# Kernel tuning notes

Measured on AMD Instinct MI355X. Metric: run time of the kernel, lower is better.

## Reference

```python
import math
import jax, jax.numpy as jnp
import numpy as np

B, S, D, H = 2, 2048, 2048, 16
HD = D // H  # 128
EPS = 1e-5


def setup_inputs() -> dict:
    key = jax.random.key(0)
    ks = jax.random.split(key, 7)
    x = jax.random.normal(ks[0], (B, S, D), jnp.float32)
    # RoPE tables: (seqlen, head_dim//2)
    theta = 10000.0
    inv_freq = 1.0 / (theta ** (np.arange(0, HD, 2, dtype=np.float32) / HD))
    t = np.arange(S, dtype=np.float32)
    freqs = np.outer(t, inv_freq)  # (S, HD//2)
    freqs_cos = jnp.asarray(np.cos(freqs), jnp.float32)
    freqs_sin = jnp.asarray(np.sin(freqs), jnp.float32)
    sc = 0.02
    wq = jax.random.normal(ks[1], (D, D), jnp.float32) * sc  # stored (in, out)
    wk = jax.random.normal(ks[2], (D, D), jnp.float32) * sc
    wv = jax.random.normal(ks[3], (D, D), jnp.float32) * sc
    wu = jax.random.normal(ks[4], (D, D), jnp.float32) * sc
    wo = jax.random.normal(ks[5], (D, D), jnp.float32) * sc
    norm_w = jnp.ones((D,), jnp.float32)
    return {"x": x, "freqs_cos": freqs_cos, "freqs_sin": freqs_sin,
            "wq": wq, "wk": wk, "wv": wv, "wu": wu, "wo": wo, "norm_w": norm_w}


def _rope(t, cos, sin):
    # t: (B, S, H, HD); cos/sin: (S, HD//2)
    tr = t.reshape(t.shape[:-1] + (-1, 2))
    r, i = tr[..., 0], tr[..., 1]
    c = cos[None, :, None, :]
    s = sin[None, :, None, :]
    out_r = r * c - i * s
    out_i = r * s + i * c
    return jnp.stack([out_r, out_i], axis=-1).reshape(t.shape)


def reference(x, freqs_cos, freqs_sin, wq, wk, wv, wu, wo, norm_w):
    b, s, d = x.shape
    h = jax.nn.silu(x)  # pre-projection SiLU on the input
    q = (h @ wq).reshape(b, s, H, HD)
    k = (h @ wk).reshape(b, s, H, HD)
    v = (h @ wv).reshape(b, s, H, HD)
    u = h @ wu  # reshape->transpose->flatten in original is identity on (b,s,d)
    q = _rope(q, freqs_cos, freqs_sin)
    k = _rope(k, freqs_cos, freqs_sin)
    # scores: (b, H, s, s)
    scores = jnp.einsum('bqhd,bkhd->bhqk', q, k) / math.sqrt(HD)
    causal = jnp.tril(jnp.ones((s, s), bool))  # mask!=0 positions zeroed; silu(0)=0
    scores = jnp.where(causal[None, None], jax.nn.silu(scores), 0.0)
    out = jnp.einsum('bhqk,bkhd->bqhd', scores, v).reshape(b, s, d)
    # RMSNorm
    out = out * jax.lax.rsqrt(jnp.mean(out * out, axis=-1, keepdims=True) + EPS)
    out = out * norm_w
    out = out * u
    return out @ wo
```

## Files before the change

### kernel.cpp

```cpp
#include <hip/hip_runtime.h>
#include <hip/hip_bf16.h>
#include <cstdint>

typedef __attribute__((ext_vector_type(8))) short bf16x8;
typedef __attribute__((ext_vector_type(4))) float f32x4;
typedef unsigned short u16;

constexpr int B = 2, S = 2048, D = 2048, H = 16, HD = 128;
constexpr int M = B * S;
constexpr int NQKU = 6144;
constexpr int ATT_LD = 3072;
constexpr float SCALE = 0.08838834764831845f;

static __device__ __forceinline__ float b2f(u16 u) {
    union { float f; uint32_t i; } v; v.i = ((uint32_t)u) << 16; return v.f;
}
static __device__ __forceinline__ u16 f2b(float f) {
    union { float f; uint32_t i; } v; v.f = f;
    uint32_t x = v.i;
    return (u16)((x + 0x7FFFu + ((x >> 16) & 1u)) >> 16);
}

__device__ __forceinline__ void gll16(const void* g, void* l) {
    __builtin_amdgcn_global_load_lds(
        (const __attribute__((address_space(1))) uint32_t*)g,
        (__attribute__((address_space(3))) uint32_t*)l, 16, 0, 0);
}

#define BAR() do { asm volatile("" ::: "memory"); __builtin_amdgcn_s_barrier(); \
                   asm volatile("" ::: "memory"); } while (0)

__global__ __launch_bounds__(256) void silu_cast(const float* __restrict__ x,
                                                 u16* __restrict__ h, int n) {
    int i = (blockIdx.x * 256 + threadIdx.x) * 4;
    if (i >= n) return;
    float4 v = *(const float4*)(x + i);
    ushort4 o;
    o.x = f2b(v.x / (1.f + __expf(-v.x)));
    o.y = f2b(v.y / (1.f + __expf(-v.y)));
    o.z = f2b(v.z / (1.f + __expf(-v.z)));
    o.w = f2b(v.w / (1.f + __expf(-v.w)));
    *(ushort4*)(h + i) = o;
}

__global__ __launch_bounds__(256) void wcast(const float* __restrict__ w,
                                             u16* __restrict__ wT) {
    __shared__ float t[64][65];
    int tx = threadIdx.x & 63, ty = threadIdx.x >> 6;
    int kb = blockIdx.y * 64, nb = blockIdx.x * 64;
    for (int r = ty; r < 64; r += 4)
        t[r][tx] = w[(size_t)(kb + r) * D + nb + tx];
    __syncthreads();
    for (int r = ty; r < 64; r += 4)
        wT[(size_t)(nb + r) * D + kb + tx] = f2b(t[tx][r]);
}

__global__ __launch_bounds__(512, 2)
void gemm_qkuv(const u16* __restrict__ A, const u16* __restrict__ BT,
               u16* __restrict__ qku, u16* __restrict__ vt) {
    __shared__ u16 lds[65536];
    const int tid = threadIdx.x;
    const int lane = tid & 63, wid = tid >> 6;
    const int wm = wid >> 2, wn = wid & 3;
    const int l16 = lane & 15, lq = lane >> 4;

    const int orig = blockIdx.x;
    const int swz = (orig & 7) * 64 + (orig >> 3);
    const int mt = swz & 15, nt = swz >> 4;
    const int m0 = mt * 256, n0 = nt * 256;

    const int srow = tid >> 2;
    const int ce = ((tid & 3) * 8) ^ (((tid >> 5) & 1) << 4);
    const int rdx = (lq * 16) ^ (((l16 >> 3) & 1) << 5);

    const u16* As0 = A + (size_t)(m0 + srow) * D + ce;
    const u16* Bs0 = BT + (size_t)(n0 + srow) * D + ce;

    {
        u16* dA = lds + wid * 512;
        u16* dB = lds + 16384 + wid * 512;
        gll16(As0,                    dA);
        gll16(As0 + (size_t)128 * D,  dA + 8192);
        gll16(Bs0,                    dB);
        gll16(Bs0 + (size_t)128 * D,  dB + 8192);
        gll16(As0 + 32,                    dA + 4096);
        gll16(As0 + 32 + (size_t)128 * D,  dA + 8192 + 4096);
        gll16(Bs0 + 32,                    dB + 4096);
        gll16(Bs0 + 32 + (size_t)128 * D,  dB + 8192 + 4096);
    }
    asm volatile("s_waitcnt vmcnt(4)" ::: "memory");
    BAR();

    f32x4 acc[8][4] = {};
    bf16x8 a[8];
    const int rbB = (wn & 1) * 4096;

#define LOAD_A(kk)                                                            \
    _Pragma("unroll") for (int mi = 0; mi < 8; ++mi)                          \
        a[mi] = *(const bf16x8*)(Abase + (kk) * 8192 +                        \
                                 (mi * 16 + l16) * 64 + rdx);
#define LOAD_B(dst, nia, kk)                                                  \
    dst = *(const bf16x8*)(Bbase + (kk) * 8192 + rbB +                        \
                           ((nia) * 16 + l16) * 64 + rdx);
#define MFMA2(n0i, n1i)                                                       \
    __builtin_amdgcn_s_setprio(1);                                            \
    _Pragma("unroll") for (int mi = 0; mi < 8; ++mi) {                        \
        acc[mi][n0i] = __builtin_amdgcn_mfma_f32_16x16x32_bf16(a[mi], b0,     \
                            acc[mi][n0i], 0, 0, 0);                           \
        acc[mi][n1i] = __builtin_amdgcn_mfma_f32_16x16x32_bf16(a[mi], b1,     \
                            acc[mi][n1i], 0, 0, 0);                           \
    }                                                                          \
    __builtin_amdgcn_s_setprio(0);

    for (int kt = 0; kt < 32; ++kt) {
        const int buf = kt & 1;
        const char* Abase = (const char*)lds + buf * 65536 + wm * 16384;
        const char* Bbase = (const char*)lds + 32768 + buf * 65536 + (wn >> 1) * 16384;
        const bool st = (kt + 1) < 32;
        const u16* Asrc = As0 + (kt + 1) * 64;
        const u16* Bsrc = Bs0 + (kt + 1) * 64;
        u16* dA = lds + (buf ^ 1) * 32768 + wid * 512;
        u16* dB = dA + 16384;
        bf16x8 b0, b1;

        LOAD_A(0);
        LOAD_B(b0, 0, 0);
        LOAD_B(b1, 1, 0);
        if (st) { gll16(Asrc, dA); gll16(Asrc + (size_t)128 * D, dA + 8192); }
        BAR();
        MFMA2(0, 1);
        BAR();
        LOAD_B(b0, 2, 0);
        LOAD_B(b1, 3, 0);
        if (st) { gll16(Bsrc, dB); gll16(Bsrc + (size_t)128 * D, dB + 8192); }
        BAR();
        MFMA2(2, 3);
        if (kt == 31) asm volatile("s_waitcnt vmcnt(0)" ::: "memory");
        else         asm volatile("s_waitcnt vmcnt(4)" ::: "memory");
        BAR();
        LOAD_A(1);
        LOAD_B(b0, 0, 1);
        LOAD_B(b1, 1, 1);
        if (st) { gll16(Asrc + 32, dA + 4096); gll16(Asrc + 32 + (size_t)128 * D, dA + 8192 + 4096); }
        BAR();
        MFMA2(0, 1);
        BAR();
        LOAD_B(b0, 2, 1);
        LOAD_B(b1, 3, 1);
        if (st) { gll16(Bsrc + 32, dB + 4096); gll16(Bsrc + 32 + (size_t)128 * D, dB + 8192 + 4096); }
        BAR();
        MFMA2(2, 3);
        if (kt < 31) asm volatile("s_waitcnt vmcnt(4)" ::: "memory");
        BAR();
    }
#undef LOAD_A
#undef LOAD_B
#undef MFMA2

    if (n0 >= NQKU) {
#pragma unroll
        for (int mi = 0; mi < 8; ++mi)
#pragma unroll
            for (int ni = 0; ni < 4; ++ni) {
                int c = n0 - NQKU + wn * 64 + ni * 16 + l16;
                int hh = c >> 7, d = c & 127;
                int row0 = m0 + wm * 128 + mi * 16 + lq * 4;
                int bb = row0 >> 11, s0 = row0 & 2047;
                ushort4 pk = make_ushort4(f2b(acc[mi][ni][0]), f2b(acc[mi][ni][1]),
                                          f2b(acc[mi][ni][2]), f2b(acc[mi][ni][3]));
                *(ushort4*)(vt + (((size_t)(bb * H + hh) * HD + d) * S + s0)) = pk;
            }
    } else {
#pragma unroll
        for (int mi = 0; mi < 8; ++mi)
#pragma unroll
            for (int ni = 0; ni < 4; ++ni)
#pragma unroll
                for (int r = 0; r < 4; ++r) {
                    int row = m0 + wm * 128 + mi * 16 + lq * 4 + r;
                    int col = n0 + wn * 64 + ni * 16 + l16;
                    qku[(size_t)row * NQKU + col] = f2b(acc[mi][ni][r]);
                }
    }
}

__global__ __launch_bounds__(256)
void gemm_bt_f32(const u16* __restrict__ A, const u16* __restrict__ BT,
                 float* __restrict__ out, int lda, int ldc, int Kk) {
    __shared__ u16 As[128 * 32];
    __shared__ u16 Bs[128 * 32];
    const int tid = threadIdx.x;
    const int lane = tid & 63, w = tid >> 6;
    const int wm = w >> 1, wn = w & 1;
    const int l16 = lane & 15, lq = lane >> 4;
    const int m0 = blockIdx.y * 128, n0 = blockIdx.x * 128;
    const int rs = lane >> 2;
    const int cs = (lane & 3) * 8;
    f32x4 acc[4][4] = {};

    const u16* Ab = A + (size_t)(m0 + w * 32 + rs) * lda + cs;
    const u16* Bb = BT + (size_t)(n0 + w * 32 + rs) * Kk + cs;
    u16* Al = As + w * 32 * 32;
    u16* Bl = Bs + w * 32 * 32;

    for (int k0 = 0; k0 < Kk; k0 += 32) {
        gll16(Ab + k0, Al);
        gll16(Ab + k0 + (size_t)16 * lda, Al + 16 * 32);
        gll16(Bb + k0, Bl);
        gll16(Bb + k0 + (size_t)16 * Kk, Bl + 16 * 32);
        __syncthreads();
        bf16x8 af[4], bfr[4];
#pragma unroll
        for (int mi = 0; mi < 4; mi++)
            af[mi] = *(const bf16x8*)(As + (wm * 64 + mi * 16 + l16) * 32 + lq * 8);
#pragma unroll
        for (int ni = 0; ni < 4; ni++)
            bfr[ni] = *(const bf16x8*)(Bs + (wn * 64 + ni * 16 + l16) * 32 + lq * 8);
#pragma unroll
        for (int mi = 0; mi < 4; mi++)
#pragma unroll
            for (int ni = 0; ni < 4; ni++)
                acc[mi][ni] = __builtin_amdgcn_mfma_f32_16x16x32_bf16(
                    af[mi], bfr[ni], acc[mi][ni], 0, 0, 0);
        __syncthreads();
    }
#pragma unroll
    for (int mi = 0; mi < 4; mi++)
#pragma unroll
        for (int ni = 0; ni < 4; ni++)
#pragma unroll
            for (int r = 0; r < 4; r++) {
                int row = m0 + wm * 64 + mi * 16 + lq * 4 + r;
                int col = n0 + wn * 64 + ni * 16 + l16;
                out[(size_t)row * ldc + col] = acc[mi][ni][r];
            }
}

__global__ __launch_bounds__(256)
void reformat(const u16* __restrict__ qku, const float* __restrict__ fc,
              const float* __restrict__ fs, u16* __restrict__ qr,
              u16* __restrict__ kr) {
    int bh = blockIdx.x;
    int s0 = blockIdx.y * 64;
    int b = bh >> 4, h = bh & 15;
    int tid = threadIdx.x;
#pragma unroll
    for (int i = 0; i < 16; ++i) {
        int p = tid + i * 256;
        int row = p >> 6, pp = p & 63;
        int sgl = s0 + row;
        float c = fc[sgl * 64 + pp], sn = fs[sgl * 64 + pp];
        size_t src = (size_t)(b * S + sgl) * NQKU + h * HD + 2 * pp;
        size_t dst = ((size_t)bh * S + sgl) * HD + 2 * pp;
        {
            uint32_t qv = *(const uint32_t*)(qku + src);
            float r = b2f((u16)(qv & 0xffff)), im = b2f((u16)(qv >> 16));
            uint32_t o = (uint32_t)f2b(r * c - im * sn) |
                         ((uint32_t)f2b(r * sn + im * c) << 16);
            *(uint32_t*)(qr + dst) = o;
        }
        {
            uint32_t kv = *(const uint32_t*)(qku + src + 2048);
            float r = b2f((u16)(kv & 0xffff)), im = b2f((u16)(kv >> 16));
            uint32_t o = (uint32_t)f2b(r * c - im * sn) |
                         ((uint32_t)f2b(r * sn + im * c) << 16);
            *(uint32_t*)(kr + dst) = o;
        }
    }
}

__global__ __launch_bounds__(512, 2)
void hstu_attn(const u16* __restrict__ qr, const u16* __restrict__ kr,
               const u16* __restrict__ vt, float* __restrict__ att) {
    __shared__ u16 k_l[16384];
    __shared__ u16 v_l[16384];
    __shared__ u16 s_l[8 * 16 * 136];
    const int bh = blockIdx.x & 31, slot = blockIdx.x >> 5;
    const int b = bh >> 4, h = bh & 15;
    const int tid = threadIdx.x, lane = tid & 63, w = tid >> 6;
    const int l16 = lane & 15, lq = lane >> 4;
    u16* s_w = s_l + w * 16 * 136;

    const u16* kb = kr + (size_t)bh * S * HD;
    const u16* vb = vt + (size_t)bh * HD * S;

    const int irow0 = tid >> 4, iu0 = tid & 15;

#define STAGE_K(k0_)                                                          \
    _Pragma("unroll") for (int r_ = 0; r_ < 4; ++r_) {                        \
        int row_ = irow0 + r_ * 32;                                           \
        int uc_ = iu0 ^ (row_ & 7);                                           \
        gll16(kb + (size_t)(k0_ + row_) * HD + uc_ * 8,                       \
              k_l + ((w * 64 + r_ * 512) << 3));                              \
    }
#define STAGE_V(k0_)                                                          \
    _Pragma("unroll") for (int r_ = 0; r_ < 4; ++r_) {                        \
        int row_ = irow0 + r_ * 32;                                           \
        int uc_ = iu0 ^ (row_ & 7);                                           \
        gll16(vb + (size_t)row_ * S + (k0_) + uc_ * 8,                        \
              v_l + ((w * 64 + r_ * 512) << 3));                              \
    }

    for (int pass = 0; pass < 2; ++pass) {
        const int t = pass ? (15 - slot) : slot;
        const int q0 = t * 128;
        const int qg0 = q0 + w * 16;

        bf16x8 qf[4];
#pragma unroll
        for (int kk = 0; kk < 4; ++kk)
            qf[kk] = *(const bf16x8*)(qr + ((size_t)bh * S + qg0 + l16) * HD +
                                      kk * 32 + lq * 8);
        f32x4 acco[8] = {};

        STAGE_K(0);
        STAGE_V(0);
        asm volatile("s_waitcnt vmcnt(0)" ::: "memory");
        BAR();

        for (int kt = 0; kt <= t; ++kt) {
            const int k0 = kt * 128;
            const bool st = kt < t;
            f32x4 accs[8] = {};
            __builtin_amdgcn_s_setprio(1);
#pragma unroll
            for (int kk = 0; kk < 4; ++kk)
#pragma unroll
                for (int ni = 0; ni < 8; ++ni) {
                    int row = ni * 16 + l16;
                    bf16x8 kf = *(const bf16x8*)(k_l + row * 128 +
                                ((kk * 32 + lq * 8) ^ ((row & 7) << 3)));
                    accs[ni] = __builtin_amdgcn_mfma_f32_16x16x32_bf16(
                        qf[kk], kf, accs[ni], 0, 0, 0);
                }
            __builtin_amdgcn_s_setprio(0);
            const bool dg = (kt == t);
#pragma unroll
            for (int ni = 0; ni < 8; ++ni)
#pragma unroll
                for (int r = 0; r < 4; ++r) {
                    int qrow = lq * 4 + r;
                    int krow = ni * 16 + l16;
                    float vv = accs[ni][r] * SCALE;
                    vv = (!dg || (k0 + krow <= qg0 + qrow))
                             ? vv / (1.f + __expf(-vv)) : 0.f;
                    s_w[qrow * 136 + krow] = f2b(vv);
                }
            BAR();
            if (st) STAGE_K(k0 + 128);
            if (st) asm volatile("s_waitcnt vmcnt(4)" ::: "memory");
            else    asm volatile("s_waitcnt vmcnt(0)" ::: "memory");
            BAR();
            __builtin_amdgcn_s_setprio(1);
#pragma unroll
            for (int kk = 0; kk < 4; ++kk) {
                bf16x8 sf = *(const bf16x8*)(s_w + l16 * 136 + kk * 32 + lq * 8);
#pragma unroll
                for (int ni = 0; ni < 8; ++ni) {
                    int row = ni * 16 + l16;
                    bf16x8 vf = *(const bf16x8*)(v_l + row * 128 +
                                ((kk * 32 + lq * 8) ^ ((row & 7) << 3)));
                    acco[ni] = __builtin_amdgcn_mfma_f32_16x16x32_bf16(
                        sf, vf, acco[ni], 0, 0, 0);
                }
            }
            __builtin_amdgcn_s_setprio(0);
            BAR();
            if (st) {
                STAGE_V(k0 + 128);
                asm volatile("s_waitcnt vmcnt(4)" ::: "memory");
            }
            BAR();
        }
#pragma unroll
        for (int ni = 0; ni < 8; ++ni)
#pragma unroll
            for (int r = 0; r < 4; ++r)
                att[(size_t)(b * S + qg0 + lq * 4 + r) * ATT_LD +
                    h * HD + ni * 16 + l16] = acco[ni][r];
    }
#undef STAGE_K
#undef STAGE_V
}

__global__ __launch_bounds__(256)
void rms_mul(const float* __restrict__ att, u16* __restrict__ qku,
             const float* __restrict__ nw) {
    int row = blockIdx.x;
    int tid = threadIdx.x;
    const float* a = att + (size_t)row * ATT_LD + tid * 8;
    float4 v0 = *(const float4*)(a);
    float4 v1 = *(const float4*)(a + 4);
    float ss = v0.x * v0.x + v0.y * v0.y + v0.z * v0.z + v0.w * v0.w +
               v1.x * v1.x + v1.y * v1.y + v1.z * v1.z + v1.w * v1.w;
#pragma unroll
    for (int off = 32; off > 0; off >>= 1) ss += __shfl_down(ss, off, 64);
    __shared__ float red[4];
    int lane = tid & 63, w = tid >> 6;
    if (lane == 0) red[w] = ss;
    __syncthreads();
    float rs = rsqrtf((red[0] + red[1] + red[2] + red[3]) * (1.f / D) + 1e-5f);
    int col = tid * 8;
    u16* up = qku + (size_t)row * NQKU + 4096 + col;
    u16 ut[8];
    *(int4*)ut = *(const int4*)up;
    float f[8] = {v0.x, v0.y, v0.z, v0.w, v1.x, v1.y, v1.z, v1.w};
    u16 o[8];
#pragma unroll
    for (int j = 0; j < 8; j++)
        o[j] = f2b(f[j] * rs * nw[col + j] * b2f(ut[j]));
    *(int4*)up = *(int4*)o;
}

extern "C" void kernel_launch(void* const* d_in, const int* in_sizes, int n_in,
                              void* d_out, int out_size, void* d_ws, size_t ws_size,
                              hipStream_t stream) {
    const float* x  = (const float*)d_in[0];
    const float* fc = (const float*)d_in[1];
    const float* fs = (const float*)d_in[2];
    const float* wq = (const float*)d_in[3];
    const float* wk = (const float*)d_in[4];
    const float* wv = (const float*)d_in[5];
    const float* wu = (const float*)d_in[6];
    const float* wo = (const float*)d_in[7];
    const float* nw = (const float*)d_in[8];
    float* out = (float*)d_out;

    char* ws = (char*)d_ws;
    const size_t WSZ = (size_t)D * D * sizeof(u16);
    u16* h_b  = (u16*)(ws);
    u16* wT   = (u16*)(ws + 2 * WSZ);
    u16* qku  = (u16*)(ws + 7 * WSZ);
    u16* vt   = (u16*)(ws + 13 * WSZ);
    u16* k_r  = (u16*)(ws + 15 * WSZ);
    u16* q_r  = h_b;
    float* att = (float*)qku;

    silu_cast<<<M * D / 1024, 256, 0, stream>>>(x, h_b, M * D);
    dim3 wg(32, 32);
    wcast<<<wg, 256, 0, stream>>>(wq, wT + 0 * (size_t)D * D);
    wcast<<<wg, 256, 0, stream>>>(wk, wT + 1 * (size_t)D * D);
    wcast<<<wg, 256, 0, stream>>>(wu, wT + 2 * (size_t)D * D);
    wcast<<<wg, 256, 0, stream>>>(wv, wT + 3 * (size_t)D * D);
    wcast<<<wg, 256, 0, stream>>>(wo, wT + 4 * (size_t)D * D);

    gemm_qkuv<<<512, 512, 0, stream>>>(h_b, wT, qku, vt);

    reformat<<<dim3(32, 32), 256, 0, stream>>>(qku, fc, fs, q_r, k_r);
    hstu_attn<<<256, 512, 0, stream>>>(q_r, k_r, vt, att);
    rms_mul<<<M, 256, 0, stream>>>(att, qku, nw);
    gemm_bt_f32<<<dim3(D / 128, M / 128), 256, 0, stream>>>(
        qku + 4096, wT + 4 * (size_t)D * D, out, NQKU, D, D);
}
```

Before: 361.7 us.

## Retile attention waves into a 2x4 grid to reuse K/V fragments

The attention kernel's per-wave work changes from 16 query rows by 128 key columns to a 2x4 wave grid. Each wave now owns 64 query rows by 32 key columns, so each K/V fragment read from LDS feeds four MFMAs instead of one, cutting LDS read traffic per tile. The score tile becomes a single block-wide shared buffer instead of per-wave slices, and SiLU uses a hardware reciprocal instead of a division. In exchange, each wave holds four times as many Q fragments in registers, which raises register pressure under the 2-blocks-per-CU launch bound and risks lower occupancy or spills.

```diff
diff --git a/kernel.cpp b/kernel.cpp
--- a/kernel.cpp
+++ b/kernel.cpp
@@ -274,16 +274,15 @@
                const u16* __restrict__ vt, float* __restrict__ att) {
     __shared__ u16 k_l[16384];
     __shared__ u16 v_l[16384];
-    __shared__ u16 s_l[8 * 16 * 136];
+    __shared__ u16 s_l[128 * 136];
     const int bh = blockIdx.x & 31, slot = blockIdx.x >> 5;
     const int b = bh >> 4, h = bh & 15;
     const int tid = threadIdx.x, lane = tid & 63, w = tid >> 6;
     const int l16 = lane & 15, lq = lane >> 4;
-    u16* s_w = s_l + w * 16 * 136;
+    const int wq = w >> 2, wk4 = w & 3;
 
     const u16* kb = kr + (size_t)bh * S * HD;
     const u16* vb = vt + (size_t)bh * HD * S;
-
     const int irow0 = tid >> 4, iu0 = tid & 15;
 
 #define STAGE_K(k0_)                                                          \
@@ -304,14 +303,16 @@
     for (int pass = 0; pass < 2; ++pass) {
         const int t = pass ? (15 - slot) : slot;
         const int q0 = t * 128;
-        const int qg0 = q0 + w * 16;
-
-        bf16x8 qf[4];
-#pragma unroll
-        for (int kk = 0; kk < 4; ++kk)
-            qf[kk] = *(const bf16x8*)(qr + ((size_t)bh * S + qg0 + l16) * HD +
-                                      kk * 32 + lq * 8);
-        f32x4 acco[8] = {};
+
+        bf16x8 qf[4][4];
+#pragma unroll
+        for (int mi = 0; mi < 4; ++mi)
+#pragma unroll
+            for (int kk = 0; kk < 4; ++kk)
+                qf[mi][kk] = *(const bf16x8*)(qr +
+                    ((size_t)bh * S + q0 + wq * 64 + mi * 16 + l16) * HD +
+                    kk * 32 + lq * 8);
+        f32x4 acco[4][2] = {};
 
         STAGE_K(0);
         STAGE_V(0);
@@ -321,31 +322,36 @@
         for (int kt = 0; kt <= t; ++kt) {
             const int k0 = kt * 128;
             const bool st = kt < t;
-            f32x4 accs[8] = {};
+            f32x4 accs[4][2] = {};
             __builtin_amdgcn_s_setprio(1);
 #pragma unroll
             for (int kk = 0; kk < 4; ++kk)
 #pragma unroll
-                for (int ni = 0; ni < 8; ++ni) {
-                    int row = ni * 16 + l16;
+                for (int ni = 0; ni < 2; ++ni) {
+                    int row = wk4 * 32 + ni * 16 + l16;
                     bf16x8 kf = *(const bf16x8*)(k_l + row * 128 +
                                 ((kk * 32 + lq * 8) ^ ((row & 7) << 3)));
-                    accs[ni] = __builtin_amdgcn_mfma_f32_16x16x32_bf16(
-                        qf[kk], kf, accs[ni], 0, 0, 0);
+#pragma unroll
+                    for (int mi = 0; mi < 4; ++mi)
+                        accs[mi][ni] = __builtin_amdgcn_mfma_f32_16x16x32_bf16(
+                            qf[mi][kk], kf, accs[mi][ni], 0, 0, 0);
                 }
             __builtin_amdgcn_s_setprio(0);
             const bool dg = (kt == t);
 #pragma unroll
-            for (int ni = 0; ni < 8; ++ni)
-#pragma unroll
-                for (int r = 0; r < 4; ++r) {
-                    int qrow = lq * 4 + r;
-                    int krow = ni * 16 + l16;
-                    float vv = accs[ni][r] * SCALE;
-                    vv = (!dg || (k0 + krow <= qg0 + qrow))
-                             ? vv / (1.f + __expf(-vv)) : 0.f;
-                    s_w[qrow * 136 + krow] = f2b(vv);
-                }
+            for (int mi = 0; mi < 4; ++mi)
+#pragma unroll
+                for (int ni = 0; ni < 2; ++ni)
+#pragma unroll
+                    for (int r = 0; r < 4; ++r) {
+                        int qrow = wq * 64 + mi * 16 + lq * 4 + r;
+                        int krow = wk4 * 32 + ni * 16 + l16;
+                        float vv = accs[mi][ni][r] * SCALE;
+                        vv = (!dg || (k0 + krow <= q0 + qrow))
+                                 ? vv * __builtin_amdgcn_rcpf(1.f + __expf(-vv))
+                                 : 0.f;
+                        s_l[qrow * 136 + krow] = f2b(vv);
+                    }
             BAR();
             if (st) STAGE_K(k0 + 128);
             if (st) asm volatile("s_waitcnt vmcnt(4)" ::: "memory");
@@ -354,14 +360,20 @@
             __builtin_amdgcn_s_setprio(1);
 #pragma unroll
             for (int kk = 0; kk < 4; ++kk) {
-                bf16x8 sf = *(const bf16x8*)(s_w + l16 * 136 + kk * 32 + lq * 8);
-#pragma unroll
-                for (int ni = 0; ni < 8; ++ni) {
-                    int row = ni * 16 + l16;
+                bf16x8 sf[4];
+#pragma unroll
+                for (int mi = 0; mi < 4; ++mi)
+                    sf[mi] = *(const bf16x8*)(s_l + (wq * 64 + mi * 16 + l16) * 136 +
+                                              kk * 32 + lq * 8);
+#pragma unroll
+                for (int ni = 0; ni < 2; ++ni) {
+                    int row = wk4 * 32 + ni * 16 + l16;
                     bf16x8 vf = *(const bf16x8*)(v_l + row * 128 +
                                 ((kk * 32 + lq * 8) ^ ((row & 7) << 3)));
-                    acco[ni] = __builtin_amdgcn_mfma_f32_16x16x32_bf16(
-                        sf, vf, acco[ni], 0, 0, 0);
+#pragma unroll
+                    for (int mi = 0; mi < 4; ++mi)
+                        acco[mi][ni] = __builtin_amdgcn_mfma_f32_16x16x32_bf16(
+                            sf[mi], vf, acco[mi][ni], 0, 0, 0);
                 }
             }
             __builtin_amdgcn_s_setprio(0);
@@ -373,11 +385,13 @@
             BAR();
         }
 #pragma unroll
-        for (int ni = 0; ni < 8; ++ni)
-#pragma unroll
-            for (int r = 0; r < 4; ++r)
-                att[(size_t)(b * S + qg0 + lq * 4 + r) * ATT_LD +
-                    h * HD + ni * 16 + l16] = acco[ni][r];
+        for (int mi = 0; mi < 4; ++mi)
+#pragma unroll
+            for (int ni = 0; ni < 2; ++ni)
+#pragma unroll
+                for (int r = 0; r < 4; ++r)
+                    att[(size_t)(b * S + q0 + wq * 64 + mi * 16 + lq * 4 + r) * ATT_LD +
+                        h * HD + wk4 * 32 + ni * 16 + l16] = acco[mi][ni][r];
     }
 #undef STAGE_K
 #undef STAGE_V
```

Result: faster. 342.5 us (-5.3%).
